# Performance work log

Hardware: AMD Instinct MI355X
Metric: run time of the kernel (lower is better)

## Reference

```python
import jax, jax.numpy as jnp
import numpy as np

B, T, CTX, D, L, H, FF, NMODES = 1024, 512, 23, 320, 5, 8, 1280, 48
DH = D // H
EPS = 1e-5


def layernorm(x, w, b):
    m = jnp.mean(x, axis=-1, keepdims=True)
    v = jnp.mean(jnp.square(x - m), axis=-1, keepdims=True)
    return (x - m) * jax.lax.rsqrt(v + EPS) * w + b


def cheb_sum(x, c):
    """sum_n c[:, n] * T_n(x) via the Chebyshev recurrence, fused with the
    reduction (Clenshaw-style accumulation, no (B,T,N+1) intermediate).
    x: (B,T) in [-1,1], c: (B, N+1)."""
    t_prev = jnp.ones_like(x)           # T_0
    t_cur = x                           # T_1
    acc = c[:, 0:1] * t_prev + c[:, 1:2] * t_cur

    def step(carry, cn):
        tp, tc, a = carry
        tn = 2.0 * x * tc - tp          # T_{n+1}
        return (tc, tn, a + cn[:, None] * tn), None

    (_, _, acc), _ = jax.lax.scan(step, (t_prev, t_cur, acc),
                                  jnp.swapaxes(c[:, 2:], 0, 1))
    return acc


def _forward(k_norm, ctx, W_e, b_e, cls, ln1_w, ln1_b, W_in, b_in, W_out, b_out,
             ln2_w, ln2_b, W1, b1, W2, b2, hln_w, hln_b, Wh1, bh1, Wh2, bh2):
    Bc = ctx.shape[0]
    # elem_proj: Linear(1, D) applied per scalar token -> (B, CTX, D)
    tok = ctx[..., None] * W_e + b_e
    x = jnp.concatenate([jnp.broadcast_to(cls, (Bc, 1, D)), tok], axis=1)  # (B, 24, D)

    def layer(x, p):
        l1w, l1b, win, bin_, wout, bout, l2w, l2b, w1, b1_, w2, b2_ = p
        # --- pre-norm self attention ---
        h = layernorm(x, l1w, l1b)
        qkv = h @ win.T + bin_                      # (B, S, 3D)
        q, k, v = jnp.split(qkv, 3, axis=-1)
        S = x.shape[1]
        q = q.reshape(Bc, S, H, DH)
        k = k.reshape(Bc, S, H, DH)
        v = v.reshape(Bc, S, H, DH)
        scores = jnp.einsum('bqhd,bkhd->bhqk', q, k) / np.sqrt(DH).astype(np.float32)
        a = jax.nn.softmax(scores, axis=-1)
        o = jnp.einsum('bhqk,bkhd->bqhd', a, v).reshape(Bc, S, D)
        x = x + o @ wout.T + bout
        # --- pre-norm FFN ---
        h2 = layernorm(x, l2w, l2b)
        x = x + jax.nn.gelu(h2 @ w1.T + b1_, approximate=False) @ w2.T + b2_
        return x, None

    x, _ = jax.lax.scan(layer, x, (ln1_w, ln1_b, W_in, b_in, W_out, b_out,
                                   ln2_w, ln2_b, W1, b1, W2, b2))
    h = layernorm(x[:, 0], hln_w, hln_b)            # CLS pooling + head LN
    c = jax.nn.gelu(h @ Wh1.T + bh1, approximate=False) @ Wh2.T + bh2  # (B, N+1)
    z = cheb_sum(k_norm, c)
    return jax.nn.sigmoid(z)


def setup_inputs() -> dict:
    key = jax.random.key(0)
    ks = jax.random.split(key, 24)
    rn = lambda k, sh, s=0.02: jax.random.normal(k, sh, jnp.float32) * s
    return {
        'k_norm': jax.random.uniform(ks[0], (B, T), jnp.float32, -1.0, 1.0),
        'ctx': jax.random.normal(ks[1], (B, CTX), jnp.float32),
        'W_e': rn(ks[2], (D,), 0.5),
        'b_e': jnp.zeros((D,), jnp.float32),
        'cls': rn(ks[3], (1, 1, D)),
        'ln1_w': jnp.ones((L, D), jnp.float32),
        'ln1_b': jnp.zeros((L, D), jnp.float32),
        'W_in': rn(ks[4], (L, 3 * D, D)),
        'b_in': jnp.zeros((L, 3 * D), jnp.float32),
        'W_out': rn(ks[5], (L, D, D)),
        'b_out': jnp.zeros((L, D), jnp.float32),
        'ln2_w': jnp.ones((L, D), jnp.float32),
        'ln2_b': jnp.zeros((L, D), jnp.float32),
        'W1': rn(ks[6], (L, FF, D)),
        'b1': jnp.zeros((L, FF), jnp.float32),
        'W2': rn(ks[7], (L, D, FF)),
        'b2': jnp.zeros((L, D), jnp.float32),
        'hln_w': jnp.ones((D,), jnp.float32),
        'hln_b': jnp.zeros((D,), jnp.float32),
        'Wh1': rn(ks[8], (D, D)),
        'bh1': jnp.zeros((D,), jnp.float32),
        'Wh2': rn(ks[9], (NMODES + 1, D)),
        'bh2': jnp.zeros((NMODES + 1,), jnp.float32),
    }


def reference(k_norm, ctx, W_e, b_e, cls, ln1_w, ln1_b, W_in, b_in, W_out, b_out,
              ln2_w, ln2_b, W1, b1, W2, b2, hln_w, hln_b, Wh1, bh1, Wh2, bh2):
    return _forward(k_norm, ctx, W_e, b_e, cls, ln1_w, ln1_b, W_in, b_in, W_out,
                    b_out, ln2_w, ln2_b, W1, b1, W2, b2, hln_w, hln_b, Wh1, bh1,
                    Wh2, bh2)
```

## Files before the change

### kernel.cpp

```cpp
#include <hip/hip_runtime.h>
#include <hip/hip_bf16.h>
#include <math.h>

#define B_SZ 1024
#define T_SZ 512
#define CTX_N 23
#define D 320
#define L_LAYERS 5
#define H 8
#define FF 1280
#define NM1 49
#define S 24
#define DH 40
#define M_ROWS (B_SZ * S)

typedef unsigned short ushort_t;
typedef __attribute__((ext_vector_type(8))) short bfrag8;
typedef __attribute__((ext_vector_type(4))) float facc4;

__device__ __forceinline__ float wave_sum(float v) {
#pragma unroll
  for (int off = 32; off > 0; off >>= 1) v += __shfl_xor(v, off, 64);
  return v;
}

__device__ __forceinline__ float gelu_exact(float x) {
  return 0.5f * x * (1.0f + erff(x * 0.70710678118654752f));
}

__device__ __forceinline__ ushort_t f2b(float x) {
  __hip_bfloat16 h = __float2bfloat16(x);
  return *reinterpret_cast<ushort_t*>(&h);
}

__device__ __forceinline__ float b2f(ushort_t u) {
  __hip_bfloat16 h = *reinterpret_cast<__hip_bfloat16*>(&u);
  return __bfloat162float(h);
}

#define GLOAD_LDS16(g, l)                                     \
  __builtin_amdgcn_global_load_lds(                           \
      (const __attribute__((address_space(1))) void*)(g),     \
      (__attribute__((address_space(3))) void*)(l), 16, 0, 0)

__global__ __launch_bounds__(256) void conv_all(
    const float* __restrict__ w_in, const float* __restrict__ w_out,
    const float* __restrict__ w1, const float* __restrict__ w2,
    const float* __restrict__ wh1, ushort_t* __restrict__ dst) {
  int i = blockIdx.x * 256 + threadIdx.x;
  const float* src;
  int off;
  if (i < 384000)       { src = w_in;  off = i; }
  else if (i < 512000)  { src = w_out; off = i - 384000; }
  else if (i < 1024000) { src = w1;    off = i - 512000; }
  else if (i < 1536000) { src = w2;    off = i - 1024000; }
  else                  { src = wh1;   off = i - 1536000; }
  float4 v = ((const float4*)src)[off];
  ushort4 o;
  o.x = f2b(v.x); o.y = f2b(v.y); o.z = f2b(v.z); o.w = f2b(v.w);
  ((ushort4*)dst)[i] = o;
}

__global__ __launch_bounds__(256) void embed_kernel(
    const float* __restrict__ ctx, const float* __restrict__ W_e,
    const float* __restrict__ b_e, const float* __restrict__ cls,
    float* __restrict__ x) {
  int idx = blockIdx.x * 256 + threadIdx.x;
  int d = idx % D;
  int s = (idx / D) % S;
  int b = idx / (D * S);
  float v;
  if (s == 0)
    v = cls[d];
  else
    v = ctx[b * CTX_N + (s - 1)] * W_e[d] + b_e[d];
  x[idx] = v;
}

__global__ __launch_bounds__(256) void ln_kernel(
    const float* __restrict__ X, const float* __restrict__ w,
    const float* __restrict__ b, ushort_t* __restrict__ Y,
    int inStride, int outStride) {
  int wv = threadIdx.x >> 6;
  int lane = threadIdx.x & 63;
  int row = blockIdx.x * 4 + wv;
  const float* xr = X + (size_t)row * inStride;
  float v[5];
#pragma unroll
  for (int i = 0; i < 5; i++) v[i] = xr[lane + 64 * i];
  float s = v[0] + v[1] + v[2] + v[3] + v[4];
  s = wave_sum(s);
  float m = s * (1.0f / (float)D);
  float sq = 0.f;
#pragma unroll
  for (int i = 0; i < 5; i++) { float d0 = v[i] - m; sq += d0 * d0; }
  sq = wave_sum(sq);
  float inv = 1.0f / sqrtf(sq * (1.0f / (float)D) + 1e-5f);
  ushort_t* yr = Y + (size_t)row * outStride;
#pragma unroll
  for (int i = 0; i < 5; i++) {
    int d = lane + 64 * i;
    yr[d] = f2b((v[i] - m) * inv * w[d] + b[d]);
  }
}

template <int EPI, int BN>
__global__ __launch_bounds__(256, 3) void gemm_mfma(
    const ushort_t* __restrict__ A, const ushort_t* __restrict__ W,
    const float* __restrict__ bias, const float* __restrict__ R,
    float* __restrict__ C, ushort_t* __restrict__ Cb, int M, int N, int K) {
  constexpr int BM = 128, BK = 64;
  constexpr int NT = BN / 32;
  constexpr int WR = BN / 32;
  __shared__ __align__(16) ushort_t As[BM * BK];
  __shared__ __align__(16) ushort_t Ws[BN * BK];

  int tid = threadIdx.x;
  int lane = tid & 63;
  int wv = tid >> 6;
  int wvM = wv & 1, wvN = wv >> 1;
  int laneM = lane & 15;
  int kgrp = lane >> 4;
  int sA = laneM & 7;
  int m0 = blockIdx.x * BM;
  int n0 = blockIdx.y * BN;

  facc4 acc[4][NT];
#pragma unroll
  for (int mt = 0; mt < 4; mt++)
#pragma unroll
    for (int nt = 0; nt < NT; nt++) acc[mt][nt] = (facc4){0.f, 0.f, 0.f, 0.f};

  int srow = tid >> 3;
  int jg = (tid & 7) ^ (srow & 7);
  const ushort_t* Ag = A + (size_t)(m0 + srow) * K + jg * 8;
  const ushort_t* Wg = W + (size_t)(n0 + srow) * K + jg * 8;

  for (int k0 = 0; k0 < K; k0 += BK) {
#pragma unroll
    for (int r = 0; r < 4; r++)
      GLOAD_LDS16(Ag + (size_t)r * 32 * K + k0, As + r * 2048 + tid * 8);
#pragma unroll
    for (int r = 0; r < WR; r++)
      GLOAD_LDS16(Wg + (size_t)r * 32 * K + k0, Ws + r * 2048 + tid * 8);
    __syncthreads();
#pragma unroll
    for (int kc = 0; kc < 2; kc++) {
      int jcol = ((kc * 4 + kgrp) ^ sA) * 8;
      bfrag8 af[4];
#pragma unroll
      for (int mt = 0; mt < 4; mt++) {
        int row = wvM * 64 + mt * 16 + laneM;
        af[mt] = *(const bfrag8*)&As[row * 64 + jcol];
      }
      bfrag8 bf[NT];
#pragma unroll
      for (int nt = 0; nt < NT; nt++) {
        int nrow = wvN * (BN / 2) + nt * 16 + laneM;
        bf[nt] = *(const bfrag8*)&Ws[nrow * 64 + jcol];
      }
#pragma unroll
      for (int mt = 0; mt < 4; mt++)
#pragma unroll
        for (int nt = 0; nt < NT; nt++)
          acc[mt][nt] = __builtin_amdgcn_mfma_f32_16x16x32_bf16(
              bf[nt], af[mt], acc[mt][nt], 0, 0, 0);
    }
    __syncthreads();
  }

#pragma unroll
  for (int mt = 0; mt < 4; mt++) {
    int m = m0 + wvM * 64 + mt * 16 + laneM;
#pragma unroll
    for (int nt = 0; nt < NT; nt++) {
      int n = n0 + wvN * (BN / 2) + nt * 16 + kgrp * 4;
      float4 bv = *(const float4*)(bias + n);
      facc4 a = acc[mt][nt];
      float v0 = a[0] + bv.x, v1 = a[1] + bv.y, v2 = a[2] + bv.z,
            v3 = a[3] + bv.w;
      size_t off = (size_t)m * N + n;
      if constexpr (EPI == 1) {
        ushort4 o;
        o.x = f2b(gelu_exact(v0)); o.y = f2b(gelu_exact(v1));
        o.z = f2b(gelu_exact(v2)); o.w = f2b(gelu_exact(v3));
        *(ushort4*)(Cb + off) = o;
      } else if constexpr (EPI == 2) {
        float4 r = *(const float4*)(R + off);
        float4 o = {v0 + r.x, v1 + r.y, v2 + r.z, v3 + r.w};
        *(float4*)(C + off) = o;
      } else if constexpr (EPI == 3) {
        float4 o = {gelu_exact(v0), gelu_exact(v1), gelu_exact(v2),
                    gelu_exact(v3)};
        *(float4*)(C + off) = o;
      } else {
        ushort4 o;
        o.x = f2b(v0); o.y = f2b(v1); o.z = f2b(v2); o.w = f2b(v3);
        *(ushort4*)(Cb + off) = o;
      }
    }
  }
}

__global__ __launch_bounds__(256) void attn_kernel(
    const ushort_t* __restrict__ qkv, ushort_t* __restrict__ o) {
  int b = blockIdx.x >> 3;
  int h = blockIdx.x & 7;
  __shared__ __align__(16) float q[S][44];
  __shared__ __align__(16) float v[S][44];
  __shared__ __align__(16) float kT[DH][28];
  __shared__ __align__(16) float sc[S][28];
  int tid = threadIdx.x;
  const ushort_t* base = qkv + (size_t)b * S * (3 * D) + h * DH;

  for (int idx = tid; idx < 720; idx += 256) {
    int t = idx / 240;
    int r = idx % 240;
    int s = r / 10, dg = r % 10;
    ushort4 u = *(const ushort4*)(base + (size_t)s * (3 * D) + t * D + dg * 4);
    float4 f = {b2f(u.x), b2f(u.y), b2f(u.z), b2f(u.w)};
    if (t == 0) {
      *(float4*)&q[s][dg * 4] = f;
    } else if (t == 2) {
      *(float4*)&v[s][dg * 4] = f;
    } else {
      kT[dg * 4 + 0][s] = f.x;
      kT[dg * 4 + 1][s] = f.y;
      kT[dg * 4 + 2][s] = f.z;
      kT[dg * 4 + 3][s] = f.w;
    }
  }
  __syncthreads();

  if (tid < 144) {
    int i = tid / 6, jg = tid % 6;
    facc4 acc = {0.f, 0.f, 0.f, 0.f};
#pragma unroll
    for (int d = 0; d < DH; d++) {
      float qv = q[i][d];
      float4 kv = *(const float4*)&kT[d][jg * 4];
      acc[0] += qv * kv.x; acc[1] += qv * kv.y;
      acc[2] += qv * kv.z; acc[3] += qv * kv.w;
    }
    const float sca = 0.15811388300841897f;
    float4 ov = {acc[0] * sca, acc[1] * sca, acc[2] * sca, acc[3] * sca};
    *(float4*)&sc[i][jg * 4] = ov;
  }
  __syncthreads();

  if (tid < S) {
    float mx = -1e30f;
#pragma unroll
    for (int j = 0; j < S; j++) mx = fmaxf(mx, sc[tid][j]);
    float sum = 0.f;
#pragma unroll
    for (int j = 0; j < S; j++) {
      float e = __expf(sc[tid][j] - mx);
      sc[tid][j] = e;
      sum += e;
    }
    float rr = 1.0f / sum;
#pragma unroll
    for (int j = 0; j < S; j++) sc[tid][j] *= rr;
  }
  __syncthreads();

  if (tid < 240) {
    int i = tid / 10, dg = tid % 10;
    facc4 acc = {0.f, 0.f, 0.f, 0.f};
#pragma unroll
    for (int j = 0; j < S; j++) {
      float p = sc[i][j];
      float4 vv = *(const float4*)&v[j][dg * 4];
      acc[0] += p * vv.x; acc[1] += p * vv.y;
      acc[2] += p * vv.z; acc[3] += p * vv.w;
    }
    ushort4 ov;
    ov.x = f2b(acc[0]); ov.y = f2b(acc[1]);
    ov.z = f2b(acc[2]); ov.w = f2b(acc[3]);
    *(ushort4*)(o + (size_t)b * S * D + (size_t)i * D + h * DH + dg * 4) = ov;
  }
}

__global__ __launch_bounds__(256) void head_cheb(
    const float* __restrict__ g, const float* __restrict__ Wh2,
    const float* __restrict__ bh2, const float* __restrict__ k_norm,
    float* __restrict__ out) {
  int b = blockIdx.x;
  __shared__ float gs[D];
  __shared__ float cs[NM1];
  int tid = threadIdx.x;
  for (int i = tid; i < D; i += 256) gs[i] = g[(size_t)b * D + i];
  __syncthreads();
  if (tid < NM1) {
    const float* wr = Wh2 + (size_t)tid * D;
    float s = bh2[tid];
    for (int d = 0; d < D; d++) s += gs[d] * wr[d];
    cs[tid] = s;
  }
  __syncthreads();
  for (int t = tid; t < T_SZ; t += 256) {
    float xv = k_norm[(size_t)b * T_SZ + t];
    float tp = 1.f, tc = xv;
    float acc = cs[0] + cs[1] * xv;
#pragma unroll
    for (int n = 2; n < NM1; n++) {
      float tn = 2.f * xv * tc - tp;
      acc += cs[n] * tn;
      tp = tc;
      tc = tn;
    }
    out[(size_t)b * T_SZ + t] = 1.f / (1.f + expf(-acc));
  }
}

extern "C" void kernel_launch(void* const* d_in, const int* in_sizes, int n_in,
                              void* d_out, int out_size, void* d_ws,
                              size_t ws_size, hipStream_t stream) {
  const float* k_norm = (const float*)d_in[0];
  const float* ctx    = (const float*)d_in[1];
  const float* W_e    = (const float*)d_in[2];
  const float* b_e    = (const float*)d_in[3];
  const float* cls    = (const float*)d_in[4];
  const float* ln1_w  = (const float*)d_in[5];
  const float* ln1_b  = (const float*)d_in[6];
  const float* W_in   = (const float*)d_in[7];
  const float* b_in   = (const float*)d_in[8];
  const float* W_out  = (const float*)d_in[9];
  const float* b_out  = (const float*)d_in[10];
  const float* ln2_w  = (const float*)d_in[11];
  const float* ln2_b  = (const float*)d_in[12];
  const float* W1     = (const float*)d_in[13];
  const float* b1     = (const float*)d_in[14];
  const float* W2     = (const float*)d_in[15];
  const float* b2     = (const float*)d_in[16];
  const float* hln_w  = (const float*)d_in[17];
  const float* hln_b  = (const float*)d_in[18];
  const float* Wh1    = (const float*)d_in[19];
  const float* bh1    = (const float*)d_in[20];
  const float* Wh2    = (const float*)d_in[21];
  const float* bh2    = (const float*)d_in[22];
  float* out = (float*)d_out;

  float* x = (float*)d_ws;
  ushort_t* hbuf = (ushort_t*)(x + (size_t)M_ROWS * D);
  ushort_t* big = hbuf + (size_t)M_ROWS * D;
  ushort_t* wb_in = big + (size_t)M_ROWS * FF;
  ushort_t* wb_out = wb_in + (size_t)L_LAYERS * 3 * D * D;
  ushort_t* wb1 = wb_out + (size_t)L_LAYERS * D * D;
  ushort_t* wb2 = wb1 + (size_t)L_LAYERS * FF * D;
  ushort_t* wbh1 = wb2 + (size_t)L_LAYERS * D * FF;
  ushort_t* hcls = wbh1 + (size_t)D * D;
  float* ghead = (float*)(hcls + (size_t)B_SZ * D);

  conv_all<<<6100, 256, 0, stream>>>(W_in, W_out, W1, W2, Wh1, wb_in);

  embed_kernel<<<(M_ROWS * D) / 256, 256, 0, stream>>>(ctx, W_e, b_e, cls, x);

  for (int l = 0; l < L_LAYERS; l++) {
    ln_kernel<<<M_ROWS / 4, 256, 0, stream>>>(x, ln1_w + l * D, ln1_b + l * D,
                                              hbuf, D, D);
    gemm_mfma<4, 160><<<dim3(M_ROWS / 128, (3 * D) / 160), 256, 0, stream>>>(
        hbuf, wb_in + (size_t)l * 3 * D * D, b_in + (size_t)l * 3 * D, nullptr,
        nullptr, big, M_ROWS, 3 * D, D);
    attn_kernel<<<B_SZ * H, 256, 0, stream>>>(big, hbuf);
    gemm_mfma<2, 160><<<dim3(M_ROWS / 128, D / 160), 256, 0, stream>>>(
        hbuf, wb_out + (size_t)l * D * D, b_out + (size_t)l * D, x, x, nullptr,
        M_ROWS, D, D);
    ln_kernel<<<M_ROWS / 4, 256, 0, stream>>>(x, ln2_w + l * D, ln2_b + l * D,
                                              hbuf, D, D);
    gemm_mfma<1, 160><<<dim3(M_ROWS / 128, FF / 160), 256, 0, stream>>>(
        hbuf, wb1 + (size_t)l * FF * D, b1 + (size_t)l * FF, nullptr, nullptr,
        big, M_ROWS, FF, D);
    gemm_mfma<2, 160><<<dim3(M_ROWS / 128, D / 160), 256, 0, stream>>>(
        big, wb2 + (size_t)l * D * FF, b2 + (size_t)l * D, x, x, nullptr,
        M_ROWS, D, FF);
  }

  ln_kernel<<<B_SZ / 4, 256, 0, stream>>>(x, hln_w, hln_b, hcls, S * D, D);
  gemm_mfma<3, 160><<<dim3(B_SZ / 128, D / 160), 256, 0, stream>>>(
      hcls, wbh1, bh1, nullptr, ghead, nullptr, B_SZ, D, D);
  head_cheb<<<B_SZ, 256, 0, stream>>>(ghead, Wh2, bh2, k_norm, out);
}
```

Measured before the change: 1.057 ms.

## Use tanh-style GELU approximation and smaller M tiles for narrow-N GEMMs

Replaces exact erf-based GELU with an exp2/rcp sigmoid-form approximation in the GEMM epilogues, cutting transcendental cost in the FF1 and head GEMMs. Also parameterizes the GEMM's M tile and uses 64-row tiles for the N=320 GEMMs (out-proj, FF2, head) to double block count and improve CU occupancy on small grids. The GELU approximation departs from the exact erf reference and may add numerical error.

```diff
diff --git a/kernel.cpp b/kernel.cpp
--- a/kernel.cpp
+++ b/kernel.cpp
@@ -24,8 +24,9 @@
   return v;
 }
 
-__device__ __forceinline__ float gelu_exact(float x) {
-  return 0.5f * x * (1.0f + erff(x * 0.70710678118654752f));
+__device__ __forceinline__ float gelu_fast(float x) {
+  float t = __builtin_amdgcn_exp2f(x * (2.30211416f + 0.10294404f * x * x));
+  return x - x * __builtin_amdgcn_rcpf(t + 1.0f);
 }
 
 __device__ __forceinline__ ushort_t f2b(float x) {
@@ -104,15 +105,17 @@
   }
 }
 
-template <int EPI, int BN>
+template <int EPI, int BM_, int NT>
 __global__ __launch_bounds__(256, 3) void gemm_mfma(
     const ushort_t* __restrict__ A, const ushort_t* __restrict__ W,
     const float* __restrict__ bias, const float* __restrict__ R,
     float* __restrict__ C, ushort_t* __restrict__ Cb, int M, int N, int K) {
-  constexpr int BM = 128, BK = 64;
-  constexpr int NT = BN / 32;
+  constexpr int BK = 64;
+  constexpr int BN = 32 * NT;
+  constexpr int MT = BM_ / 32;
+  constexpr int AR = BM_ / 32;
   constexpr int WR = BN / 32;
-  __shared__ __align__(16) ushort_t As[BM * BK];
+  __shared__ __align__(16) ushort_t As[BM_ * BK];
   __shared__ __align__(16) ushort_t Ws[BN * BK];
 
   int tid = threadIdx.x;
@@ -122,12 +125,12 @@
   int laneM = lane & 15;
   int kgrp = lane >> 4;
   int sA = laneM & 7;
-  int m0 = blockIdx.x * BM;
+  int m0 = blockIdx.x * BM_;
   int n0 = blockIdx.y * BN;
 
-  facc4 acc[4][NT];
-#pragma unroll
-  for (int mt = 0; mt < 4; mt++)
+  facc4 acc[MT][NT];
+#pragma unroll
+  for (int mt = 0; mt < MT; mt++)
 #pragma unroll
     for (int nt = 0; nt < NT; nt++) acc[mt][nt] = (facc4){0.f, 0.f, 0.f, 0.f};
 
@@ -138,7 +141,7 @@
 
   for (int k0 = 0; k0 < K; k0 += BK) {
 #pragma unroll
-    for (int r = 0; r < 4; r++)
+    for (int r = 0; r < AR; r++)
       GLOAD_LDS16(Ag + (size_t)r * 32 * K + k0, As + r * 2048 + tid * 8);
 #pragma unroll
     for (int r = 0; r < WR; r++)
@@ -147,10 +150,10 @@
 #pragma unroll
     for (int kc = 0; kc < 2; kc++) {
       int jcol = ((kc * 4 + kgrp) ^ sA) * 8;
-      bfrag8 af[4];
-#pragma unroll
-      for (int mt = 0; mt < 4; mt++) {
-        int row = wvM * 64 + mt * 16 + laneM;
+      bfrag8 af[MT];
+#pragma unroll
+      for (int mt = 0; mt < MT; mt++) {
+        int row = wvM * (BM_ / 2) + mt * 16 + laneM;
         af[mt] = *(const bfrag8*)&As[row * 64 + jcol];
       }
       bfrag8 bf[NT];
@@ -160,7 +163,7 @@
         bf[nt] = *(const bfrag8*)&Ws[nrow * 64 + jcol];
       }
 #pragma unroll
-      for (int mt = 0; mt < 4; mt++)
+      for (int mt = 0; mt < MT; mt++)
 #pragma unroll
         for (int nt = 0; nt < NT; nt++)
           acc[mt][nt] = __builtin_amdgcn_mfma_f32_16x16x32_bf16(
@@ -170,8 +173,8 @@
   }
 
 #pragma unroll
-  for (int mt = 0; mt < 4; mt++) {
-    int m = m0 + wvM * 64 + mt * 16 + laneM;
+  for (int mt = 0; mt < MT; mt++) {
+    int m = m0 + wvM * (BM_ / 2) + mt * 16 + laneM;
 #pragma unroll
     for (int nt = 0; nt < NT; nt++) {
       int n = n0 + wvN * (BN / 2) + nt * 16 + kgrp * 4;
@@ -182,16 +185,16 @@
       size_t off = (size_t)m * N + n;
       if constexpr (EPI == 1) {
         ushort4 o;
-        o.x = f2b(gelu_exact(v0)); o.y = f2b(gelu_exact(v1));
-        o.z = f2b(gelu_exact(v2)); o.w = f2b(gelu_exact(v3));
+        o.x = f2b(gelu_fast(v0)); o.y = f2b(gelu_fast(v1));
+        o.z = f2b(gelu_fast(v2)); o.w = f2b(gelu_fast(v3));
         *(ushort4*)(Cb + off) = o;
       } else if constexpr (EPI == 2) {
         float4 r = *(const float4*)(R + off);
         float4 o = {v0 + r.x, v1 + r.y, v2 + r.z, v3 + r.w};
         *(float4*)(C + off) = o;
       } else if constexpr (EPI == 3) {
-        float4 o = {gelu_exact(v0), gelu_exact(v1), gelu_exact(v2),
-                    gelu_exact(v3)};
+        float4 o = {gelu_fast(v0), gelu_fast(v1), gelu_fast(v2),
+                    gelu_fast(v3)};
         *(float4*)(C + off) = o;
       } else {
         ushort4 o;
@@ -360,25 +363,26 @@
   for (int l = 0; l < L_LAYERS; l++) {
     ln_kernel<<<M_ROWS / 4, 256, 0, stream>>>(x, ln1_w + l * D, ln1_b + l * D,
                                               hbuf, D, D);
-    gemm_mfma<4, 160><<<dim3(M_ROWS / 128, (3 * D) / 160), 256, 0, stream>>>(
+    gemm_mfma<4, 128, 5><<<dim3(M_ROWS / 128, (3 * D) / 160), 256, 0,
+                           stream>>>(
         hbuf, wb_in + (size_t)l * 3 * D * D, b_in + (size_t)l * 3 * D, nullptr,
         nullptr, big, M_ROWS, 3 * D, D);
     attn_kernel<<<B_SZ * H, 256, 0, stream>>>(big, hbuf);
-    gemm_mfma<2, 160><<<dim3(M_ROWS / 128, D / 160), 256, 0, stream>>>(
+    gemm_mfma<2, 64, 5><<<dim3(M_ROWS / 64, D / 160), 256, 0, stream>>>(
         hbuf, wb_out + (size_t)l * D * D, b_out + (size_t)l * D, x, x, nullptr,
         M_ROWS, D, D);
     ln_kernel<<<M_ROWS / 4, 256, 0, stream>>>(x, ln2_w + l * D, ln2_b + l * D,
                                               hbuf, D, D);
-    gemm_mfma<1, 160><<<dim3(M_ROWS / 128, FF / 160), 256, 0, stream>>>(
+    gemm_mfma<1, 128, 5><<<dim3(M_ROWS / 128, FF / 160), 256, 0, stream>>>(
         hbuf, wb1 + (size_t)l * FF * D, b1 + (size_t)l * FF, nullptr, nullptr,
         big, M_ROWS, FF, D);
-    gemm_mfma<2, 160><<<dim3(M_ROWS / 128, D / 160), 256, 0, stream>>>(
+    gemm_mfma<2, 64, 5><<<dim3(M_ROWS / 64, D / 160), 256, 0, stream>>>(
         big, wb2 + (size_t)l * D * FF, b2 + (size_t)l * D, x, x, nullptr,
         M_ROWS, D, FF);
   }
 
   ln_kernel<<<B_SZ / 4, 256, 0, stream>>>(x, hln_w, hln_b, hcls, S * D, D);
-  gemm_mfma<3, 160><<<dim3(B_SZ / 128, D / 160), 256, 0, stream>>>(
+  gemm_mfma<3, 64, 5><<<dim3(B_SZ / 64, D / 160), 256, 0, stream>>>(
       hcls, wbh1, bh1, nullptr, ghead, nullptr, B_SZ, D, D);
   head_cheb<<<B_SZ, 256, 0, stream>>>(ghead, Wh2, bh2, k_norm, out);
 }
```

Result: faster. 1.020 ms (-3.5%).
